# Optimization experiments

Hardware: AMD Instinct MI355X
Metric: run time of the kernel (lower is better)

## Reference

```python
import jax, jax.numpy as jnp
import numpy as np

B, S, E = 4, 2048, 1024


def setup_inputs() -> dict:
    key = jax.random.key(0)
    k1, k2, k3, k4 = jax.random.split(key, 4)
    scale = 1.0 / np.sqrt(E)
    return {
        "x": jax.random.normal(k1, (B, S, E), dtype=jnp.float32),
        "W_Q": jax.random.normal(k2, (E, E), dtype=jnp.float32) * scale,
        "W_K": jax.random.normal(k3, (E, E), dtype=jnp.float32) * scale,
        "W_V": jax.random.normal(k4, (E, E), dtype=jnp.float32) * scale,
    }


def reference(x, W_Q, W_K, W_V):
    # nn.Linear(E, E, bias=False): y = x @ W.T
    Q = jnp.einsum("bse,fe->bsf", x, W_Q)
    K = jnp.einsum("bse,fe->bsf", x, W_K)
    V = jnp.einsum("bse,fe->bsf", x, W_V)
    d = Q.shape[-1]
    scores = jnp.einsum("bqd,bkd->bqk", Q, K) / jnp.sqrt(jnp.float32(d))
    # causal mask: -inf strictly above the diagonal
    seq = Q.shape[1]
    causal = jnp.tril(jnp.ones((seq, seq), dtype=bool))  # [S,S]
    scores = jnp.where(causal[None, :, :], scores, jnp.float32(-jnp.inf))
    attn = jax.nn.softmax(scores, axis=-1)
    return jnp.einsum("bqk,bkd->bqd", attn, V)
```

## Files before the change

### kernel.cpp

```cpp
#include <hip/hip_runtime.h>
#include <hip/hip_bf16.h>
#include <stdint.h>

typedef __hip_bfloat16 bf16;
typedef __attribute__((ext_vector_type(8))) short bf16x8;
typedef __attribute__((ext_vector_type(4))) float f32x4;
typedef __attribute__((ext_vector_type(8))) unsigned short u16x8;
typedef __attribute__((ext_vector_type(4))) unsigned short u16x4;

#define SLEN 2048
#define ED   1024
#define NB   4
#define AS1 __attribute__((address_space(1)))
#define AS3 __attribute__((address_space(3)))

static __device__ __forceinline__ unsigned short f2bf(float f) {
    return __builtin_bit_cast(unsigned short, __float2bfloat16(f));
}

__device__ __forceinline__ void gemm_core(
    const char* __restrict__ aT, int lda,
    const char* __restrict__ bT, int ldb,
    int nkt, char* sm, int tid, f32x4 (&acc)[4][4])
{
    const int lane = tid & 63, wave = tid >> 6;
    const int wm = wave >> 1, wn = wave & 1;
    const int fr = lane & 15, kc = lane >> 4;

    auto STAGE = [&](int kh, int Tn) {
        char* buf = sm + (Tn & 1) * 49152;
#pragma unroll
        for (int j = 0; j < 2; ++j) {
            int rid = j * 512 + tid;
            int row = rid >> 2, c = rid & 3;
            const char* src = aT + (size_t)row * lda + Tn * 128 + kh * 64
                            + ((c ^ ((row >> 1) & 3)) * 16);
            __builtin_amdgcn_global_load_lds(
                (const AS1 uint32_t*)src,
                (AS3 uint32_t*)(buf + kh * 16384 + (j * 512 + wave * 64) * 16),
                16, 0, 0);
        }
        {
            int row = tid >> 2, c = tid & 3;
            const char* src = bT + (size_t)row * ldb + Tn * 128 + kh * 64
                            + ((c ^ ((row >> 1) & 3)) * 16);
            __builtin_amdgcn_global_load_lds(
                (const AS1 uint32_t*)src,
                (AS3 uint32_t*)(buf + 32768 + kh * 8192 + (wave * 64) * 16),
                16, 0, 0);
        }
    };

    STAGE(0, 0); STAGE(1, 0);
    asm volatile("s_waitcnt vmcnt(3)" ::: "memory");
    __builtin_amdgcn_sched_barrier(0);
    __builtin_amdgcn_s_barrier();

    for (int T = 0; T < nkt; ++T) {
        const bool pre = (T + 1 < nkt);
        const char* buf = sm + (T & 1) * 49152;
#pragma unroll
        for (int kh = 0; kh < 2; ++kh) {
            bf16x8 a[4], b[4];
#pragma unroll
            for (int i = 0; i < 4; ++i) {
                int row = wm * 64 + i * 16 + fr;
                a[i] = *(const bf16x8*)(buf + kh * 16384 + row * 64
                                        + ((kc ^ ((row >> 1) & 3)) * 16));
            }
#pragma unroll
            for (int i = 0; i < 4; ++i) {
                int row = wn * 64 + i * 16 + fr;
                b[i] = *(const bf16x8*)(buf + 32768 + kh * 8192 + row * 64
                                        + ((kc ^ ((row >> 1) & 3)) * 16));
            }
            if (pre) {
                STAGE(kh, T + 1);
                asm volatile("s_waitcnt vmcnt(3)" ::: "memory");
            } else {
                asm volatile("s_waitcnt vmcnt(0)" ::: "memory");
            }
            __builtin_amdgcn_sched_barrier(0);
            __builtin_amdgcn_s_barrier();
            asm volatile("s_waitcnt lgkmcnt(0)" ::: "memory");
            __builtin_amdgcn_sched_barrier(0);
            __builtin_amdgcn_s_setprio(1);
#pragma unroll
            for (int i = 0; i < 4; ++i)
#pragma unroll
                for (int n = 0; n < 4; ++n)
                    acc[i][n] = __builtin_amdgcn_mfma_f32_16x16x32_bf16(
                        a[i], b[n], acc[i][n], 0, 0, 0);
            __builtin_amdgcn_s_setprio(0);
            __builtin_amdgcn_s_barrier();
        }
    }
}

__global__ __launch_bounds__(256) void convert_to_bf16(
    const float* __restrict__ x, const float* __restrict__ wq,
    const float* __restrict__ wk, const float* __restrict__ wv,
    bf16* __restrict__ xb, bf16* __restrict__ wqb,
    bf16* __restrict__ wkb, bf16* __restrict__ wvb)
{
    long g = (long)blockIdx.x * 256 + threadIdx.x;
    const float* src; bf16* dst; long o;
    if (g < 1048576) { src = x; dst = xb; o = g * 8; }
    else {
        long g2 = g - 1048576;
        int w = (int)(g2 >> 17);
        o = (g2 & 131071) * 8;
        src = (w == 0) ? wq : (w == 1) ? wk : wv;
        dst = (w == 0) ? wqb : (w == 1) ? wkb : wvb;
    }
    float4 v0 = *(const float4*)(src + o);
    float4 v1 = *(const float4*)(src + o + 4);
    u16x8 r;
    r[0] = f2bf(v0.x); r[1] = f2bf(v0.y); r[2] = f2bf(v0.z); r[3] = f2bf(v0.w);
    r[4] = f2bf(v1.x); r[5] = f2bf(v1.y); r[6] = f2bf(v1.z); r[7] = f2bf(v1.w);
    *(u16x8*)(dst + o) = r;
}

__global__ __launch_bounds__(512, 2) void qkv_gemm(
    const bf16* __restrict__ xb, const bf16* __restrict__ wqb,
    const bf16* __restrict__ wkb, const bf16* __restrict__ wvb,
    bf16* __restrict__ Qb, bf16* __restrict__ Kb, bf16* __restrict__ Vt)
{
    extern __shared__ char smem[];
    int bid = blockIdx.x, tid = threadIdx.x;
    int xcd = bid & 7, i = bid >> 3;
    int tm = (xcd << 2) | (i & 3);
    int tn = i >> 2;
    const bf16* W = (tn < 8) ? wqb : (tn < 16) ? wkb : wvb;
    int tnl = tn & 7;
    f32x4 acc[4][4] = {};
    gemm_core((const char*)(xb + (size_t)tm * 256 * ED), ED * 2,
              (const char*)(W + (size_t)tnl * 128 * ED), ED * 2,
              16, smem, tid, acc);

    int lane = tid & 63, wave = tid >> 6, wm = wave >> 1, wn = wave & 1;
    int rl = (lane >> 4) * 4, cl = lane & 15;
    if (tn < 16) {
        bf16* C = (tn < 8) ? Qb : Kb;
#pragma unroll
        for (int mf = 0; mf < 4; ++mf)
#pragma unroll
            for (int j = 0; j < 4; ++j) {
                int r = tm * 256 + wm * 64 + mf * 16 + rl + j;
#pragma unroll
                for (int nf = 0; nf < 4; ++nf) {
                    int c = tnl * 128 + wn * 64 + nf * 16 + cl;
                    C[(size_t)r * ED + c] = __float2bfloat16(acc[mf][nf][j]);
                }
            }
    } else {
#pragma unroll
        for (int mf = 0; mf < 4; ++mf)
#pragma unroll
            for (int j = 0; j < 4; ++j) {
                int r = tm * 256 + wm * 64 + mf * 16 + rl + j;
                int bb = r >> 11, s = r & 2047;
#pragma unroll
                for (int nf = 0; nf < 4; ++nf) {
                    int d = tnl * 128 + wn * 64 + nf * 16 + cl;
                    Vt[(((size_t)bb << 10) + d) * SLEN + s] = __float2bfloat16(acc[mf][nf][j]);
                }
            }
    }
}

__global__ __launch_bounds__(512, 2) void qk_gemm(
    const bf16* __restrict__ Qb, const bf16* __restrict__ Kb, float* __restrict__ Sc)
{
    extern __shared__ char smem[];
    int bx = blockIdx.x, b = blockIdx.y, tid = threadIdx.x;
    int t = (bx & 7) * 9 + (bx >> 3);
    int ti = 0;
    while ((ti + 1) * (ti + 2) <= t) ++ti;
    int tj = t - ti * (ti + 1);
    f32x4 acc[4][4] = {};
    gemm_core((const char*)(Qb + ((size_t)b * SLEN + ti * 256) * ED), ED * 2,
              (const char*)(Kb + ((size_t)b * SLEN + tj * 128) * ED), ED * 2,
              16, smem, tid, acc);

    float* Sb = Sc + (size_t)b * SLEN * SLEN;
    int lane = tid & 63, wave = tid >> 6, wm = wave >> 1, wn = wave & 1;
    int rl = (lane >> 4) * 4, cl = lane & 15;
#pragma unroll
    for (int mf = 0; mf < 4; ++mf)
#pragma unroll
        for (int j = 0; j < 4; ++j) {
            int r = ti * 256 + wm * 64 + mf * 16 + rl + j;
#pragma unroll
            for (int nf = 0; nf < 4; ++nf) {
                int c = tj * 128 + wn * 64 + nf * 16 + cl;
                Sb[(size_t)r * SLEN + c] = acc[mf][nf][j] * 0.03125f;
            }
        }
}

__global__ __launch_bounds__(256) void softmax_rows(float* __restrict__ Sc)
{
    int q = blockIdx.x, b = blockIdx.y, tid = threadIdx.x;
    float* row = Sc + ((size_t)b * SLEN + q) * SLEN;
    int lane = tid & 63, wave = tid >> 6;
    __shared__ float red[4];

    float vals[8];
    float lmax = -3.0e38f;
#pragma unroll
    for (int r = 0; r < 2; ++r) {
        int i4 = tid + r * 256;
        if (i4 * 4 <= q) {
            float4 v = *(const float4*)(row + i4 * 4);
            vals[r * 4 + 0] = v.x; vals[r * 4 + 1] = v.y;
            vals[r * 4 + 2] = v.z; vals[r * 4 + 3] = v.w;
#pragma unroll
            for (int e = 0; e < 4; ++e) {
                int k = i4 * 4 + e;
                if (k <= q) lmax = fmaxf(lmax, vals[r * 4 + e]);
            }
        }
    }
#pragma unroll
    for (int o = 32; o > 0; o >>= 1) lmax = fmaxf(lmax, __shfl_xor(lmax, o));
    if (lane == 0) red[wave] = lmax;
    __syncthreads();
    float m = fmaxf(fmaxf(red[0], red[1]), fmaxf(red[2], red[3]));
    __syncthreads();
    float lsum = 0.f;
#pragma unroll
    for (int r = 0; r < 2; ++r) {
        int i4 = tid + r * 256;
        if (i4 * 4 <= q)
#pragma unroll
            for (int e = 0; e < 4; ++e) {
                int k = i4 * 4 + e;
                if (k <= q) lsum += __expf(vals[r * 4 + e] - m);
            }
    }
#pragma unroll
    for (int o = 32; o > 0; o >>= 1) lsum += __shfl_xor(lsum, o);
    if (lane == 0) red[wave] = lsum;
    __syncthreads();
    float inv = 1.0f / (red[0] + red[1] + red[2] + red[3]);
    unsigned short* prow = (unsigned short*)row;
#pragma unroll
    for (int r = 0; r < 2; ++r) {
        int i4 = tid + r * 256;
        u16x4 o4;
#pragma unroll
        for (int e = 0; e < 4; ++e) {
            int k = i4 * 4 + e;
            float p = (k <= q) ? __expf(vals[r * 4 + e] - m) * inv : 0.0f;
            o4[e] = f2bf(p);
        }
        *(u16x4*)(prow + i4 * 4) = o4;
    }
}

__global__ __launch_bounds__(512, 2) void pv_gemm(
    const bf16* __restrict__ P, const bf16* __restrict__ Vt, float* __restrict__ O)
{
    extern __shared__ char smem[];
    int mq = 7 - blockIdx.x, nd = blockIdx.y, b = blockIdx.z, tid = threadIdx.x;
    f32x4 acc[4][4] = {};
    int nkt = (mq + 1) * 4;
    gemm_core((const char*)P + ((size_t)b * SLEN + mq * 256) * 8192, 8192,
              (const char*)(Vt + ((size_t)b * ED + nd * 128) * SLEN), SLEN * 2,
              nkt, smem, tid, acc);

    int lane = tid & 63, wave = tid >> 6, wm = wave >> 1, wn = wave & 1;
    int rl = (lane >> 4) * 4, cl = lane & 15;
    float* Ob = O + (size_t)b * SLEN * ED;
#pragma unroll
    for (int mf = 0; mf < 4; ++mf)
#pragma unroll
        for (int j = 0; j < 4; ++j) {
            int r = mq * 256 + wm * 64 + mf * 16 + rl + j;
#pragma unroll
            for (int nf = 0; nf < 4; ++nf) {
                int c = nd * 128 + wn * 64 + nf * 16 + cl;
                Ob[(size_t)r * ED + c] = acc[mf][nf][j];
            }
        }
}

extern "C" void kernel_launch(void* const* d_in, const int* in_sizes, int n_in,
                              void* d_out, int out_size, void* d_ws, size_t ws_size,
                              hipStream_t stream)
{
    const float* x  = (const float*)d_in[0];
    const float* wq = (const float*)d_in[1];
    const float* wk = (const float*)d_in[2];
    const float* wv = (const float*)d_in[3];
    float* out = (float*)d_out;

    char* ws = (char*)d_ws;
    bf16* xb  = (bf16*)(ws);
    bf16* wqb = (bf16*)(ws + 16777216);
    bf16* wkb = (bf16*)(ws + 18874368);
    bf16* wvb = (bf16*)(ws + 20971520);
    bf16* Qb  = (bf16*)(ws + 23068672);
    bf16* Kb  = (bf16*)(ws + 39845888);
    bf16* Vt  = (bf16*)(ws + 56623104);
    float* Sc = (float*)(ws + 73400320);

    (void)hipFuncSetAttribute((const void*)qkv_gemm,
            hipFuncAttributeMaxDynamicSharedMemorySize, 98304);
    (void)hipFuncSetAttribute((const void*)qk_gemm,
            hipFuncAttributeMaxDynamicSharedMemorySize, 98304);
    (void)hipFuncSetAttribute((const void*)pv_gemm,
            hipFuncAttributeMaxDynamicSharedMemorySize, 98304);

    convert_to_bf16<<<5632, 256, 0, stream>>>(x, wq, wk, wv, xb, wqb, wkb, wvb);
    qkv_gemm<<<768, 512, 98304, stream>>>(xb, wqb, wkb, wvb, Qb, Kb, Vt);
    qk_gemm<<<dim3(72, NB), 512, 98304, stream>>>(Qb, Kb, Sc);
    softmax_rows<<<dim3(SLEN, NB), 256, 0, stream>>>(Sc);
    pv_gemm<<<dim3(8, 8, NB), 512, 98304, stream>>>((const bf16*)Sc, Vt, out);
}
```

Measured before the change: 168.6 us.

## Software-pipeline LDS fragment reads with MFMA using double register sets

Restructures the GEMM inner loop so that the LDS fragment reads for the next k-half are issued before the MFMAs of the previous k-half run. Two register sets (even and odd) alternate, and partial lgkmcnt waits let shared-memory loads overlap with matrix math. This cuts one barrier per k-half and hides LDS latency. In exchange it uses more VGPRs for the extra fragments and depends on careful counting of the waitcnt values.

```diff
diff --git a/kernel.cpp b/kernel.cpp
--- a/kernel.cpp
+++ b/kernel.cpp
@@ -13,6 +13,7 @@
 #define NB   4
 #define AS1 __attribute__((address_space(1)))
 #define AS3 __attribute__((address_space(3)))
+#define SB0() __builtin_amdgcn_sched_barrier(0)
 
 static __device__ __forceinline__ unsigned short f2bf(float f) {
     return __builtin_bit_cast(unsigned short, __float2bfloat16(f));
@@ -50,51 +51,68 @@
                 16, 0, 0);
         }
     };
+    auto RD = [&](int T, int kh, bf16x8 (&a)[4], bf16x8 (&b)[4]) {
+        const char* buf = sm + (T & 1) * 49152;
+#pragma unroll
+        for (int i = 0; i < 4; ++i) {
+            int row = wm * 64 + i * 16 + fr;
+            a[i] = *(const bf16x8*)(buf + kh * 16384 + row * 64
+                                    + ((kc ^ ((row >> 1) & 3)) * 16));
+        }
+#pragma unroll
+        for (int i = 0; i < 4; ++i) {
+            int row = wn * 64 + i * 16 + fr;
+            b[i] = *(const bf16x8*)(buf + 32768 + kh * 8192 + row * 64
+                                    + ((kc ^ ((row >> 1) & 3)) * 16));
+        }
+    };
+    auto MM = [&](bf16x8 (&a)[4], bf16x8 (&b)[4]) {
+        __builtin_amdgcn_s_setprio(1);
+#pragma unroll
+        for (int i = 0; i < 4; ++i)
+#pragma unroll
+            for (int n = 0; n < 4; ++n)
+                acc[i][n] = __builtin_amdgcn_mfma_f32_16x16x32_bf16(
+                    a[i], b[n], acc[i][n], 0, 0, 0);
+        __builtin_amdgcn_s_setprio(0);
+    };
 
     STAGE(0, 0); STAGE(1, 0);
     asm volatile("s_waitcnt vmcnt(3)" ::: "memory");
-    __builtin_amdgcn_sched_barrier(0);
+    SB0();
     __builtin_amdgcn_s_barrier();
 
+    bf16x8 aE[4], bE[4], aO[4], bO[4];
     for (int T = 0; T < nkt; ++T) {
         const bool pre = (T + 1 < nkt);
-        const char* buf = sm + (T & 1) * 49152;
-#pragma unroll
-        for (int kh = 0; kh < 2; ++kh) {
-            bf16x8 a[4], b[4];
-#pragma unroll
-            for (int i = 0; i < 4; ++i) {
-                int row = wm * 64 + i * 16 + fr;
-                a[i] = *(const bf16x8*)(buf + kh * 16384 + row * 64
-                                        + ((kc ^ ((row >> 1) & 3)) * 16));
-            }
-#pragma unroll
-            for (int i = 0; i < 4; ++i) {
-                int row = wn * 64 + i * 16 + fr;
-                b[i] = *(const bf16x8*)(buf + 32768 + kh * 8192 + row * 64
-                                        + ((kc ^ ((row >> 1) & 3)) * 16));
-            }
-            if (pre) {
-                STAGE(kh, T + 1);
-                asm volatile("s_waitcnt vmcnt(3)" ::: "memory");
-            } else {
-                asm volatile("s_waitcnt vmcnt(0)" ::: "memory");
-            }
-            __builtin_amdgcn_sched_barrier(0);
-            __builtin_amdgcn_s_barrier();
-            asm volatile("s_waitcnt lgkmcnt(0)" ::: "memory");
-            __builtin_amdgcn_sched_barrier(0);
-            __builtin_amdgcn_s_setprio(1);
-#pragma unroll
-            for (int i = 0; i < 4; ++i)
-#pragma unroll
-                for (int n = 0; n < 4; ++n)
-                    acc[i][n] = __builtin_amdgcn_mfma_f32_16x16x32_bf16(
-                        a[i], b[n], acc[i][n], 0, 0, 0);
-            __builtin_amdgcn_s_setprio(0);
-            __builtin_amdgcn_s_barrier();
-        }
-    }
+        RD(T, 0, aE, bE);
+        SB0();
+        if (pre) STAGE(0, T + 1);
+        SB0();
+        if (T > 0) {
+            asm volatile("s_waitcnt lgkmcnt(8)" ::: "memory");
+            SB0();
+            MM(aO, bO);
+        }
+        if (pre) asm volatile("s_waitcnt vmcnt(3)" ::: "memory");
+        else     asm volatile("s_waitcnt vmcnt(0)" ::: "memory");
+        SB0();
+        __builtin_amdgcn_s_barrier();
+        RD(T, 1, aO, bO);
+        SB0();
+        if (pre) STAGE(1, T + 1);
+        SB0();
+        asm volatile("s_waitcnt lgkmcnt(8)" ::: "memory");
+        SB0();
+        MM(aE, bE);
+        if (pre) asm volatile("s_waitcnt vmcnt(3)" ::: "memory");
+        else     asm volatile("s_waitcnt vmcnt(0)" ::: "memory");
+        SB0();
+        __builtin_amdgcn_s_barrier();
+    }
+    asm volatile("s_waitcnt lgkmcnt(0)" ::: "memory");
+    SB0();
+    MM(aO, bO);
 }
 
 __global__ __launch_bounds__(256) void convert_to_bf16(
```

Result: faster. 155.1 us (-8.0%).
